# Optimization experiments

Measured on AMD Instinct MI355X. Metric: run time of the kernel, lower is better.

Reference implementation:

```python
import jax, jax.numpy as jnp
import numpy as np
from jax import lax

G = 32          # growthrate / num_features
KS = 3          # filter_size
PAD = (KS - 1) // 2
NUM_LAYERS = 4


def _conv2d(x, w, b):
    # x: [B, Cin, H, W], w: [Cout, Cin, k, k]
    y = lax.conv_general_dilated(
        x, w, window_strides=(1, 1), padding=[(PAD, PAD), (PAD, PAD)],
        dimension_numbers=("NCHW", "OIHW", "NCHW"))
    return y + b[None, :, None, None]


def _scan_cell(xs, w, b):
    # xs: [T, B, Cin, H, W]; ConvLSTM-like cell: A = tanh(conv(cat(x, c)))
    # split A -> (ai[G], af[G], ao[1]); h = ai; c_next = sigmoid(ao) * af
    T, B, _, H, W = xs.shape
    c0 = jnp.zeros((B, G, H, W), xs.dtype)

    def step(c, x):
        A = jnp.tanh(_conv2d(jnp.concatenate([x, c], axis=1), w, b))
        h = A[:, :G]
        cand = A[:, G:2 * G]
        gate = jax.nn.sigmoid(A[:, 2 * G:])
        c_next = gate * cand
        return c_next, (h, c_next, gate)

    _, (hs, cs, gs) = lax.scan(step, c0, xs)
    return hs, cs, gs  # each [T, B, G or 1, H, W]


def setup_inputs() -> dict:
    key = jax.random.key(0)
    ks = jax.random.split(key, 1 + 4 * NUM_LAYERS)
    T, B, C, H, W = 8, 4, 32, 64, 64
    inp = {"x": jax.random.normal(ks[0], (T, B, C, H, W), jnp.float32)}
    cin = [C] + [2 * l * G for l in range(1, NUM_LAYERS)]  # [32, 64, 128, 192]
    cout = 2 * G + 1
    for l in range(NUM_LAYERS):
        ci = cin[l] + G
        inp[f"wf{l}"] = jax.random.normal(ks[1 + 4 * l], (cout, ci, KS, KS), jnp.float32) * 0.02
        inp[f"bf{l}"] = jax.random.normal(ks[2 + 4 * l], (cout,), jnp.float32) * 0.02
        inp[f"wb{l}"] = jax.random.normal(ks[3 + 4 * l], (cout, ci, KS, KS), jnp.float32) * 0.02
        inp[f"bb{l}"] = jax.random.normal(ks[4 + 4 * l], (cout,), jnp.float32) * 0.02
    return inp


def reference(x, wf0, bf0, wb0, bb0, wf1, bf1, wb1, bb1,
              wf2, bf2, wb2, bb2, wf3, bf3, wb3, bb3):
    fwd = [(wf0, bf0), (wf1, bf1), (wf2, bf2), (wf3, bf3)]
    bwd = [(wb0, bb0), (wb1, bb1), (wb2, bb2), (wb3, bb3)]
    output = x  # [T, B, C, H, W]
    lr_h, lr_c, lr_g = [], [], []
    for l in range(NUM_LAYERS):
        hf, cf, gf = _scan_cell(output, *fwd[l])
        hb, _, _ = _scan_cell(output[::-1], *bwd[l])
        hb = hb[::-1]  # align backward pass to original time order
        cur = jnp.concatenate([hf, hb], axis=2)  # [T, B, 2G, H, W]
        output = cur if l == 0 else jnp.concatenate([output, cur], axis=2)
        lr_h.append(hf[-1]); lr_c.append(cf[-1]); lr_g.append(gf[-1])
    return (output, jnp.stack(lr_h), jnp.stack(lr_c), jnp.stack(lr_g))
```

## Files before the change

### kernel.cpp

```cpp
#include <hip/hip_runtime.h>
#include <math.h>

#define T_STEPS 8
#define HW 4096
#define XSTR 192
#define FR_ROW 4352

typedef unsigned short u16;
typedef __attribute__((ext_vector_type(8))) short short8;
typedef __attribute__((ext_vector_type(4))) short short4v;
typedef __attribute__((ext_vector_type(4))) float f32x4;

__device__ __forceinline__ u16 f2bf(float f) {
    unsigned u = __builtin_bit_cast(unsigned, f);
    u += 0x7fffu + ((u >> 16) & 1u);
    return (u16)(u >> 16);
}
__device__ __forceinline__ float bf2f(u16 h) {
    unsigned u = ((unsigned)h) << 16;
    return __builtin_bit_cast(float, u);
}
__device__ __forceinline__ float ftanh(float x) {
    float e = __expf(2.f * x);
    return 1.f - 2.f * __builtin_amdgcn_rcpf(e + 1.f);
}
__device__ __forceinline__ float fsigm(float x) {
    return __builtin_amdgcn_rcpf(1.f + __expf(-x));
}

__global__ __launch_bounds__(256) void transpose_halo(
    const float* __restrict__ src, u16* __restrict__ XT, int src_ctot)
{
    __shared__ float tile[32][257];
    const int img = blockIdx.z;
    const int px0 = blockIdx.x * 256;
    const float* s = src + (size_t)img * src_ctot * HW + px0;
    #pragma unroll
    for (int c = 0; c < 32; ++c)
        tile[c][threadIdx.x] = s[(size_t)c * HW + threadIdx.x];
    __syncthreads();
    const int c = threadIdx.x & 31, pb = threadIdx.x >> 5;
    const int r0 = px0 >> 6;
    for (int p = pb; p < 256; p += 8) {
        int row = r0 + (p >> 6), col = p & 63;
        XT[((size_t)img * 4356 + (row + 1) * 66 + col + 1) * XSTR + c] = f2bf(tile[c][p]);
    }
}

__global__ __launch_bounds__(256) void prep_w(
    const float* __restrict__ wf, const float* __restrict__ wb,
    u16* __restrict__ Wr, int ci_total)
{
    int idx = blockIdx.x * 256 + threadIdx.x;
    int total = 2 * 9 * 80 * ci_total;
    if (idx >= total) return;
    int ci = idx % ci_total;
    int rest = idx / ci_total;
    int co = rest % 80; rest /= 80;
    int tap = rest % 9;
    int dir = rest / 9;
    const float* w = dir ? wb : wf;
    float v = (co < 65) ? w[((size_t)co * ci_total + ci) * 9 + tap] : 0.f;
    Wr[idx] = f2bf(v);
}

__global__ __launch_bounds__(512, 2) void convx_mfma(
    const u16* __restrict__ XT, const u16* __restrict__ Wr,
    const float* __restrict__ b_f, const float* __restrict__ b_b,
    u16* __restrict__ convx, int cin, int ci_total)
{
    __shared__ u16 xs[6 * 66 * 32];
    const int tid = threadIdx.x;
    const int l = tid & 63, wv = tid >> 6;
    const int g = l >> 4, ln16 = l & 15;
    const int img = blockIdx.z;
    const int dir = wv & 1;
    const int wrow = wv >> 1;
    const int r0  = blockIdx.x * 4;
    const int orow = r0 + wrow;

    const float* bias = dir ? b_b : b_f;
    f32x4 acc[5][4];
    #pragma unroll
    for (int mt = 0; mt < 5; ++mt)
        #pragma unroll
        for (int r = 0; r < 4; ++r) {
            int co = mt * 16 + g * 4 + r;
            float bv = (co < 65) ? bias[co] : 0.f;
            #pragma unroll
            for (int nt = 0; nt < 4; ++nt) acc[mt][nt][r] = bv;
        }

    const u16* wdir = Wr + (size_t)dir * 9 * 80 * ci_total + g * 8;
    const u16* xim  = XT + (size_t)img * 4356 * XSTR;

    for (int ch = 0; ch < cin; ch += 32) {
        __syncthreads();
        #pragma unroll
        for (int k = 0; k < 4; ++k) {
            int idx = k * 512 + tid;
            if (idx < 1584) {
                int seg = idx & 3;
                int pr  = idx >> 2;
                short8 v = *(const short8*)(xim + (size_t)(r0 * 66 + pr) * XSTR + ch + seg * 8);
                *(short8*)(xs + (size_t)idx * 8) = v;
            }
        }
        __syncthreads();

        #pragma unroll
        for (int ky = 0; ky < 3; ++ky) {
            #pragma unroll
            for (int kx = 0; kx < 3; ++kx) {
                const int tap = ky * 3 + kx;
                const u16* xb = xs + ((size_t)((wrow + ky) * 66 + ln16 + kx)) * 32 + g * 8;
                short8 bv0 = *(const short8*)(xb);
                short8 bv1 = *(const short8*)(xb + 16 * 32);
                short8 bv2 = *(const short8*)(xb + 32 * 32);
                short8 bv3 = *(const short8*)(xb + 48 * 32);
                const u16* wb_ = wdir + ((size_t)tap * 80 + ln16) * ci_total + ch;
                #pragma unroll
                for (int mt = 0; mt < 5; ++mt) {
                    short8 af = *(const short8*)(wb_ + (size_t)mt * 16 * ci_total);
                    acc[mt][0] = __builtin_amdgcn_mfma_f32_16x16x32_bf16(af, bv0, acc[mt][0], 0, 0, 0);
                    acc[mt][1] = __builtin_amdgcn_mfma_f32_16x16x32_bf16(af, bv1, acc[mt][1], 0, 0, 0);
                    acc[mt][2] = __builtin_amdgcn_mfma_f32_16x16x32_bf16(af, bv2, acc[mt][2], 0, 0, 0);
                    acc[mt][3] = __builtin_amdgcn_mfma_f32_16x16x32_bf16(af, bv3, acc[mt][3], 0, 0, 0);
                }
            }
        }
    }

    const int zimg = dir * 32 + img;
    u16* cb = convx + ((size_t)zimg * 64 + orow) * FR_ROW;
    #pragma unroll
    for (int mt = 0; mt < 4; ++mt)
        #pragma unroll
        for (int nt = 0; nt < 4; ++nt) {
            short4v pk;
            #pragma unroll
            for (int r = 0; r < 4; ++r) pk[r] = (short)f2bf(acc[mt][nt][r]);
            *(short4v*)(cb + (size_t)(nt * 4 + mt) * 256 + l * 4) = pk;
        }
    if (g == 0) {
        #pragma unroll
        for (int nt = 0; nt < 4; ++nt) {
            short4v pk;
            #pragma unroll
            for (int r = 0; r < 4; ++r) pk[r] = (short)f2bf(acc[4][nt][r]);
            *(short4v*)(cb + 4096 + nt * 64 + ln16 * 4) = pk;
        }
    }
}

__global__ __launch_bounds__(256) void rec_mfma(
    const u16* __restrict__ cT_in, u16* __restrict__ cT_out,
    const u16* __restrict__ Wr, const u16* __restrict__ convx,
    float* __restrict__ out_t,
    float* __restrict__ lrh, float* __restrict__ lrc, float* __restrict__ lrg,
    u16* __restrict__ XT,
    int cin, int ci_total, int layer, int step)
{
    const int tid = threadIdx.x;
    const int l = tid & 63, wv = tid >> 6;
    const int g = l >> 4, ln16 = l & 15;
    const int z = blockIdx.z;
    const int dir = z >> 2, b = z & 3;
    const int t = dir ? (7 - step) : step;
    const int row  = blockIdx.x * 2 + (wv >> 1);
    const int nb   = (wv & 1) * 2;
    const int col0 = nb * 16;

    const int zimg = dir * 32 + t * 4 + b;
    const u16* cxb = convx + ((size_t)zimg * 64 + row) * FR_ROW;
    f32x4 acc[5][2];
    #pragma unroll
    for (int mt = 0; mt < 4; ++mt)
        #pragma unroll
        for (int nt = 0; nt < 2; ++nt) {
            short4v pk = *(const short4v*)(cxb + (size_t)((nb + nt) * 4 + mt) * 256 + l * 4);
            #pragma unroll
            for (int r = 0; r < 4; ++r) acc[mt][nt][r] = bf2f((u16)pk[r]);
        }
    #pragma unroll
    for (int nt = 0; nt < 2; ++nt) {
        if (g == 0) {
            short4v pk = *(const short4v*)(cxb + 4096 + (nb + nt) * 64 + ln16 * 4);
            #pragma unroll
            for (int r = 0; r < 4; ++r) acc[4][nt][r] = bf2f((u16)pk[r]);
        } else {
            #pragma unroll
            for (int r = 0; r < 4; ++r) acc[4][nt][r] = 0.f;
        }
    }

    const u16* wdir = Wr + (size_t)dir * 9 * 80 * ci_total + cin + g * 8;
    const u16* cim  = cT_in + (size_t)z * 4356 * 32 + g * 8;

    #pragma unroll
    for (int ky = 0; ky < 3; ++ky) {
        #pragma unroll
        for (int kx = 0; kx < 3; ++kx) {
            const int tap = ky * 3 + kx;
            const u16* xb_ = cim + (size_t)((row + ky) * 66 + col0 + ln16 + kx) * 32;
            short8 bv0 = *(const short8*)(xb_);
            short8 bv1 = *(const short8*)(xb_ + 16 * 32);
            const u16* wb_ = wdir + ((size_t)tap * 80 + ln16) * ci_total;
            #pragma unroll
            for (int mt = 0; mt < 5; ++mt) {
                short8 af = *(const short8*)(wb_ + (size_t)mt * 16 * ci_total);
                acc[mt][0] = __builtin_amdgcn_mfma_f32_16x16x32_bf16(af, bv0, acc[mt][0], 0, 0, 0);
                acc[mt][1] = __builtin_amdgcn_mfma_f32_16x16x32_bf16(af, bv1, acc[mt][1], 0, 0, 0);
            }
        }
    }

    const bool last_f = (dir == 0) && (step == 7);
    float val[2], gv[2];
    #pragma unroll
    for (int nt = 0; nt < 2; ++nt) {
        val[nt] = fsigm(ftanh(acc[4][nt][0]));
        gv[nt]  = __shfl(val[nt], ln16);
    }

    const size_t obase = (size_t)(t * 4 + b) * 256 + 64 * layer + dir * 32;
    const int chb = 64 * layer + dir * 32;
    #pragma unroll
    for (int mt = 0; mt < 2; ++mt)
        #pragma unroll
        for (int nt = 0; nt < 2; ++nt) {
            int px = row * 64 + col0 + nt * 16 + ln16;
            short4v pkh;
            #pragma unroll
            for (int r = 0; r < 4; ++r) {
                int co = mt * 16 + g * 4 + r;
                float v = ftanh(acc[mt][nt][r]);
                out_t[(obase + co) * HW + px] = v;
                pkh[r] = (short)f2bf(v);
                if (last_f) lrh[((size_t)(layer * 4 + b) * 32 + co) * HW + px] = v;
            }
            if (layer < 3)
                *(short4v*)(XT + ((size_t)(t * 4 + b) * 4356 + (row + 1) * 66 +
                                  (col0 + nt * 16 + ln16 + 1)) * XSTR + chb + mt * 16 + g * 4) = pkh;
        }
    #pragma unroll
    for (int mt = 2; mt < 4; ++mt)
        #pragma unroll
        for (int nt = 0; nt < 2; ++nt) {
            short4v pk;
            #pragma unroll
            for (int r = 0; r < 4; ++r) {
                int k = (mt - 2) * 16 + g * 4 + r;
                float c = gv[nt] * ftanh(acc[mt][nt][r]);
                pk[r] = (short)f2bf(c);
                if (last_f)
                    lrc[((size_t)(layer * 4 + b) * 32 + k) * HW + row * 64 + col0 + nt * 16 + ln16] = c;
            }
            int colh = col0 + nt * 16 + ln16 + 1;
            *(short4v*)(cT_out + ((size_t)z * 4356 + (row + 1) * 66 + colh) * 32 + (mt - 2) * 16 + g * 4) = pk;
        }
    if (last_f && g == 0) {
        #pragma unroll
        for (int nt = 0; nt < 2; ++nt)
            lrg[(size_t)(layer * 4 + b) * HW + row * 64 + col0 + nt * 16 + ln16] = val[nt];
    }
}

extern "C" void kernel_launch(void* const* d_in, const int* in_sizes, int n_in,
                              void* d_out, int out_size, void* d_ws, size_t ws_size,
                              hipStream_t stream)
{
    const float* x = (const float*)d_in[0];
    float* out = (float*)d_out;
    float* lrh = out + (size_t)33554432;
    float* lrc = lrh + (size_t)2097152;
    float* lrg = lrc + (size_t)2097152;

    char* ws = (char*)d_ws;
    u16* convx = (u16*)ws;
    size_t off = 35651584 + 4096;
    u16* cT_a = (u16*)(ws + off); off += 2230272;
    u16* cT_b = (u16*)(ws + off); off += 2230272;
    u16* XT   = (u16*)(ws + off); off += 53526528;
    u16* Wr   = (u16*)(ws + off);

    hipMemsetAsync(XT, 0, 53526528, stream);
    hipMemsetAsync(cT_b, 0, 2230272, stream);
    transpose_halo<<<dim3(16, 1, 32), 256, 0, stream>>>(x, XT, 32);

    for (int l = 0; l < 4; ++l) {
        const float* wf = (const float*)d_in[1 + 4 * l];
        const float* bf = (const float*)d_in[2 + 4 * l];
        const float* wb = (const float*)d_in[3 + 4 * l];
        const float* bb = (const float*)d_in[4 + 4 * l];
        int cin = (l == 0) ? 32 : 64 * l;
        int ci_total = cin + 32;

        prep_w<<<dim3((2 * 9 * 80 * ci_total + 255) / 256), 256, 0, stream>>>(wf, wb, Wr, ci_total);
        convx_mfma<<<dim3(16, 1, 32), 512, 0, stream>>>(XT, Wr, bf, bb, convx, cin, ci_total);

        hipMemsetAsync(cT_a, 0, 2230272, stream);
        for (int s = 0; s < 8; ++s) {
            const u16* cin_p = (s & 1) ? cT_b : cT_a;
            u16* cout_p      = (s & 1) ? cT_a : cT_b;
            rec_mfma<<<dim3(32, 1, 8), 256, 0, stream>>>(
                cin_p, cout_p, Wr, convx, out, lrh, lrc, lrg, XT, cin, ci_total, l, s);
        }
    }
}
```

Baseline: 616.4 us.

## Batch weight prep, stage two channel chunks per sync, split rec work across waves

```diff
diff --git a/kernel.cpp b/kernel.cpp
--- a/kernel.cpp
+++ b/kernel.cpp
@@ -47,19 +47,24 @@
     }
 }
 
-__global__ __launch_bounds__(256) void prep_w(
-    const float* __restrict__ wf, const float* __restrict__ wb,
-    u16* __restrict__ Wr, int ci_total)
+struct WP { const float* p[8]; };
+
+__global__ __launch_bounds__(256) void prep_w_all(WP wp, u16* __restrict__ Wr)
 {
     int idx = blockIdx.x * 256 + threadIdx.x;
-    int total = 2 * 9 * 80 * ci_total;
-    if (idx >= total) return;
-    int ci = idx % ci_total;
-    int rest = idx / ci_total;
+    if (idx >= 783360) return;
+    const int offs[5] = {0, 92160, 230400, 460800, 783360};
+    const int cit[4]  = {64, 96, 160, 224};
+    int lay = 0;
+    while (idx >= offs[lay + 1]) ++lay;
+    int li = idx - offs[lay];
+    int ci_total = cit[lay];
+    int ci = li % ci_total;
+    int rest = li / ci_total;
     int co = rest % 80; rest /= 80;
     int tap = rest % 9;
     int dir = rest / 9;
-    const float* w = dir ? wb : wf;
+    const float* w = wp.p[lay * 2 + dir];
     float v = (co < 65) ? w[((size_t)co * ci_total + ci) * 9 + tap] : 0.f;
     Wr[idx] = f2bf(v);
 }
@@ -69,7 +74,7 @@
     const float* __restrict__ b_f, const float* __restrict__ b_b,
     u16* __restrict__ convx, int cin, int ci_total)
 {
-    __shared__ u16 xs[6 * 66 * 32];
+    __shared__ u16 xs[2][6 * 66 * 32];
     const int tid = threadIdx.x;
     const int l = tid & 63, wv = tid >> 6;
     const int g = l >> 4, ln16 = l & 15;
@@ -93,39 +98,47 @@
 
     const u16* wdir = Wr + (size_t)dir * 9 * 80 * ci_total + g * 8;
     const u16* xim  = XT + (size_t)img * 4356 * XSTR;
-
-    for (int ch = 0; ch < cin; ch += 32) {
+    const int nstage = (cin >= 64) ? 3168 : 1584;
+
+    for (int ch0 = 0; ch0 < cin; ch0 += 64) {
         __syncthreads();
         #pragma unroll
-        for (int k = 0; k < 4; ++k) {
+        for (int k = 0; k < 7; ++k) {
             int idx = k * 512 + tid;
-            if (idx < 1584) {
-                int seg = idx & 3;
-                int pr  = idx >> 2;
-                short8 v = *(const short8*)(xim + (size_t)(r0 * 66 + pr) * XSTR + ch + seg * 8);
-                *(short8*)(xs + (size_t)idx * 8) = v;
+            if (idx < nstage) {
+                int bufi = (idx >= 1584) ? 1 : 0;
+                int ii = idx - bufi * 1584;
+                int seg = ii & 3, pr = ii >> 2;
+                short8 v = *(const short8*)(xim + (size_t)(r0 * 66 + pr) * XSTR
+                                            + ch0 + bufi * 32 + seg * 8);
+                *(short8*)(xs[bufi] + (size_t)ii * 8) = v;
             }
         }
         __syncthreads();
 
         #pragma unroll
-        for (int ky = 0; ky < 3; ++ky) {
-            #pragma unroll
-            for (int kx = 0; kx < 3; ++kx) {
-                const int tap = ky * 3 + kx;
-                const u16* xb = xs + ((size_t)((wrow + ky) * 66 + ln16 + kx)) * 32 + g * 8;
-                short8 bv0 = *(const short8*)(xb);
-                short8 bv1 = *(const short8*)(xb + 16 * 32);
-                short8 bv2 = *(const short8*)(xb + 32 * 32);
-                short8 bv3 = *(const short8*)(xb + 48 * 32);
-                const u16* wb_ = wdir + ((size_t)tap * 80 + ln16) * ci_total + ch;
+        for (int cc = 0; cc < 2; ++cc) {
+            const int ch = ch0 + cc * 32;
+            if (ch >= cin) break;
+            #pragma unroll
+            for (int ky = 0; ky < 3; ++ky) {
                 #pragma unroll
-                for (int mt = 0; mt < 5; ++mt) {
-                    short8 af = *(const short8*)(wb_ + (size_t)mt * 16 * ci_total);
-                    acc[mt][0] = __builtin_amdgcn_mfma_f32_16x16x32_bf16(af, bv0, acc[mt][0], 0, 0, 0);
-                    acc[mt][1] = __builtin_amdgcn_mfma_f32_16x16x32_bf16(af, bv1, acc[mt][1], 0, 0, 0);
-                    acc[mt][2] = __builtin_amdgcn_mfma_f32_16x16x32_bf16(af, bv2, acc[mt][2], 0, 0, 0);
-                    acc[mt][3] = __builtin_amdgcn_mfma_f32_16x16x32_bf16(af, bv3, acc[mt][3], 0, 0, 0);
+                for (int kx = 0; kx < 3; ++kx) {
+                    const int tap = ky * 3 + kx;
+                    const u16* xb = xs[cc] + ((size_t)((wrow + ky) * 66 + ln16 + kx)) * 32 + g * 8;
+                    short8 bv0 = *(const short8*)(xb);
+                    short8 bv1 = *(const short8*)(xb + 16 * 32);
+                    short8 bv2 = *(const short8*)(xb + 32 * 32);
+                    short8 bv3 = *(const short8*)(xb + 48 * 32);
+                    const u16* wb_ = wdir + ((size_t)tap * 80 + ln16) * ci_total + ch;
+                    #pragma unroll
+                    for (int mt = 0; mt < 5; ++mt) {
+                        short8 af = *(const short8*)(wb_ + (size_t)mt * 16 * ci_total);
+                        acc[mt][0] = __builtin_amdgcn_mfma_f32_16x16x32_bf16(af, bv0, acc[mt][0], 0, 0, 0);
+                        acc[mt][1] = __builtin_amdgcn_mfma_f32_16x16x32_bf16(af, bv1, acc[mt][1], 0, 0, 0);
+                        acc[mt][2] = __builtin_amdgcn_mfma_f32_16x16x32_bf16(af, bv2, acc[mt][2], 0, 0, 0);
+                        acc[mt][3] = __builtin_amdgcn_mfma_f32_16x16x32_bf16(af, bv3, acc[mt][3], 0, 0, 0);
+                    }
                 }
             }
         }
@@ -153,7 +166,7 @@
     }
 }
 
-__global__ __launch_bounds__(256) void rec_mfma(
+__global__ __launch_bounds__(512) void rec_mfma(
     const u16* __restrict__ cT_in, u16* __restrict__ cT_out,
     const u16* __restrict__ Wr, const u16* __restrict__ convx,
     float* __restrict__ out_t,
@@ -162,107 +175,118 @@
     int cin, int ci_total, int layer, int step)
 {
     const int tid = threadIdx.x;
-    const int l = tid & 63, wv = tid >> 6;
+    const int l = tid & 63, w = tid >> 6;
     const int g = l >> 4, ln16 = l & 15;
+    const int role = w & 1, ws = w >> 1;
     const int z = blockIdx.z;
     const int dir = z >> 2, b = z & 3;
     const int t = dir ? (7 - step) : step;
-    const int row  = blockIdx.x * 2 + (wv >> 1);
-    const int nb   = (wv & 1) * 2;
+    const int row  = blockIdx.x * 2 + (ws >> 1);
+    const int nb   = (ws & 1) * 2;
     const int col0 = nb * 16;
-
     const int zimg = dir * 32 + t * 4 + b;
+    const int m0 = role * 2;
+
     const u16* cxb = convx + ((size_t)zimg * 64 + row) * FR_ROW;
-    f32x4 acc[5][2];
-    #pragma unroll
-    for (int mt = 0; mt < 4; ++mt)
+    f32x4 acc[3][2];
+    #pragma unroll
+    for (int j = 0; j < 2; ++j)
         #pragma unroll
         for (int nt = 0; nt < 2; ++nt) {
-            short4v pk = *(const short4v*)(cxb + (size_t)((nb + nt) * 4 + mt) * 256 + l * 4);
-            #pragma unroll
-            for (int r = 0; r < 4; ++r) acc[mt][nt][r] = bf2f((u16)pk[r]);
+            short4v pk = *(const short4v*)(cxb + (size_t)((nb + nt) * 4 + (m0 + j)) * 256 + l * 4);
+            #pragma unroll
+            for (int r = 0; r < 4; ++r) acc[j][nt][r] = bf2f((u16)pk[r]);
         }
     #pragma unroll
     for (int nt = 0; nt < 2; ++nt) {
         if (g == 0) {
             short4v pk = *(const short4v*)(cxb + 4096 + (nb + nt) * 64 + ln16 * 4);
             #pragma unroll
-            for (int r = 0; r < 4; ++r) acc[4][nt][r] = bf2f((u16)pk[r]);
+            for (int r = 0; r < 4; ++r) acc[2][nt][r] = bf2f((u16)pk[r]);
         } else {
             #pragma unroll
-            for (int r = 0; r < 4; ++r) acc[4][nt][r] = 0.f;
-        }
-    }
-
-    const u16* wdir = Wr + (size_t)dir * 9 * 80 * ci_total + cin + g * 8;
-    const u16* cim  = cT_in + (size_t)z * 4356 * 32 + g * 8;
-
-    #pragma unroll
-    for (int ky = 0; ky < 3; ++ky) {
-        #pragma unroll
-        for (int kx = 0; kx < 3; ++kx) {
-            const int tap = ky * 3 + kx;
-            const u16* xb_ = cim + (size_t)((row + ky) * 66 + col0 + ln16 + kx) * 32;
-            short8 bv0 = *(const short8*)(xb_);
-            short8 bv1 = *(const short8*)(xb_ + 16 * 32);
-            const u16* wb_ = wdir + ((size_t)tap * 80 + ln16) * ci_total;
-            #pragma unroll
-            for (int mt = 0; mt < 5; ++mt) {
-                short8 af = *(const short8*)(wb_ + (size_t)mt * 16 * ci_total);
-                acc[mt][0] = __builtin_amdgcn_mfma_f32_16x16x32_bf16(af, bv0, acc[mt][0], 0, 0, 0);
-                acc[mt][1] = __builtin_amdgcn_mfma_f32_16x16x32_bf16(af, bv1, acc[mt][1], 0, 0, 0);
-            }
-        }
+            for (int r = 0; r < 4; ++r) acc[2][nt][r] = 0.f;
+        }
+    }
+
+    if (step > 0) {
+        const u16* wdir = Wr + (size_t)dir * 9 * 80 * ci_total + cin + g * 8;
+        const u16* cim  = cT_in + (size_t)z * 4356 * 32 + g * 8;
+        __builtin_amdgcn_s_setprio(1);
+        #pragma unroll
+        for (int ky = 0; ky < 3; ++ky) {
+            #pragma unroll
+            for (int kx = 0; kx < 3; ++kx) {
+                const int tap = ky * 3 + kx;
+                const u16* xb_ = cim + (size_t)((row + ky) * 66 + col0 + ln16 + kx) * 32;
+                short8 bv0 = *(const short8*)(xb_);
+                short8 bv1 = *(const short8*)(xb_ + 16 * 32);
+                const u16* wb_ = wdir + ((size_t)tap * 80 + ln16) * ci_total;
+                short8 af0 = *(const short8*)(wb_ + (size_t)(m0    ) * 16 * ci_total);
+                short8 af1 = *(const short8*)(wb_ + (size_t)(m0 + 1) * 16 * ci_total);
+                short8 af4 = *(const short8*)(wb_ + (size_t)4 * 16 * ci_total);
+                acc[0][0] = __builtin_amdgcn_mfma_f32_16x16x32_bf16(af0, bv0, acc[0][0], 0, 0, 0);
+                acc[0][1] = __builtin_amdgcn_mfma_f32_16x16x32_bf16(af0, bv1, acc[0][1], 0, 0, 0);
+                acc[1][0] = __builtin_amdgcn_mfma_f32_16x16x32_bf16(af1, bv0, acc[1][0], 0, 0, 0);
+                acc[1][1] = __builtin_amdgcn_mfma_f32_16x16x32_bf16(af1, bv1, acc[1][1], 0, 0, 0);
+                acc[2][0] = __builtin_amdgcn_mfma_f32_16x16x32_bf16(af4, bv0, acc[2][0], 0, 0, 0);
+                acc[2][1] = __builtin_amdgcn_mfma_f32_16x16x32_bf16(af4, bv1, acc[2][1], 0, 0, 0);
+            }
+        }
+        __builtin_amdgcn_s_setprio(0);
     }
 
     const bool last_f = (dir == 0) && (step == 7);
     float val[2], gv[2];
     #pragma unroll
     for (int nt = 0; nt < 2; ++nt) {
-        val[nt] = fsigm(ftanh(acc[4][nt][0]));
+        val[nt] = fsigm(ftanh(acc[2][nt][0]));
         gv[nt]  = __shfl(val[nt], ln16);
     }
 
-    const size_t obase = (size_t)(t * 4 + b) * 256 + 64 * layer + dir * 32;
-    const int chb = 64 * layer + dir * 32;
-    #pragma unroll
-    for (int mt = 0; mt < 2; ++mt)
-        #pragma unroll
-        for (int nt = 0; nt < 2; ++nt) {
-            int px = row * 64 + col0 + nt * 16 + ln16;
-            short4v pkh;
-            #pragma unroll
-            for (int r = 0; r < 4; ++r) {
-                int co = mt * 16 + g * 4 + r;
-                float v = ftanh(acc[mt][nt][r]);
-                out_t[(obase + co) * HW + px] = v;
-                pkh[r] = (short)f2bf(v);
-                if (last_f) lrh[((size_t)(layer * 4 + b) * 32 + co) * HW + px] = v;
-            }
-            if (layer < 3)
-                *(short4v*)(XT + ((size_t)(t * 4 + b) * 4356 + (row + 1) * 66 +
-                                  (col0 + nt * 16 + ln16 + 1)) * XSTR + chb + mt * 16 + g * 4) = pkh;
-        }
-    #pragma unroll
-    for (int mt = 2; mt < 4; ++mt)
-        #pragma unroll
-        for (int nt = 0; nt < 2; ++nt) {
-            short4v pk;
-            #pragma unroll
-            for (int r = 0; r < 4; ++r) {
-                int k = (mt - 2) * 16 + g * 4 + r;
-                float c = gv[nt] * ftanh(acc[mt][nt][r]);
-                pk[r] = (short)f2bf(c);
-                if (last_f)
-                    lrc[((size_t)(layer * 4 + b) * 32 + k) * HW + row * 64 + col0 + nt * 16 + ln16] = c;
-            }
-            int colh = col0 + nt * 16 + ln16 + 1;
-            *(short4v*)(cT_out + ((size_t)z * 4356 + (row + 1) * 66 + colh) * 32 + (mt - 2) * 16 + g * 4) = pk;
-        }
-    if (last_f && g == 0) {
-        #pragma unroll
-        for (int nt = 0; nt < 2; ++nt)
-            lrg[(size_t)(layer * 4 + b) * HW + row * 64 + col0 + nt * 16 + ln16] = val[nt];
+    if (role == 0) {
+        const size_t obase = (size_t)(t * 4 + b) * 256 + 64 * layer + dir * 32;
+        const int chb = 64 * layer + dir * 32;
+        #pragma unroll
+        for (int j = 0; j < 2; ++j)
+            #pragma unroll
+            for (int nt = 0; nt < 2; ++nt) {
+                int px = row * 64 + col0 + nt * 16 + ln16;
+                short4v pkh;
+                #pragma unroll
+                for (int r = 0; r < 4; ++r) {
+                    int co = j * 16 + g * 4 + r;
+                    float v = ftanh(acc[j][nt][r]);
+                    out_t[(obase + co) * HW + px] = v;
+                    pkh[r] = (short)f2bf(v);
+                    if (last_f) lrh[((size_t)(layer * 4 + b) * 32 + co) * HW + px] = v;
+                }
+                if (layer < 3)
+                    *(short4v*)(XT + ((size_t)(t * 4 + b) * 4356 + (row + 1) * 66 +
+                                      (col0 + nt * 16 + ln16 + 1)) * XSTR + chb + j * 16 + g * 4) = pkh;
+            }
+        if (last_f && g == 0) {
+            #pragma unroll
+            for (int nt = 0; nt < 2; ++nt)
+                lrg[(size_t)(layer * 4 + b) * HW + row * 64 + col0 + nt * 16 + ln16] = val[nt];
+        }
+    } else {
+        #pragma unroll
+        for (int j = 0; j < 2; ++j)
+            #pragma unroll
+            for (int nt = 0; nt < 2; ++nt) {
+                short4v pk;
+                #pragma unroll
+                for (int r = 0; r < 4; ++r) {
+                    int k = j * 16 + g * 4 + r;
+                    float c = gv[nt] * ftanh(acc[j][nt][r]);
+                    pk[r] = (short)f2bf(c);
+                    if (last_f)
+                        lrc[((size_t)(layer * 4 + b) * 32 + k) * HW + row * 64 + col0 + nt * 16 + ln16] = c;
+                }
+                int colh = col0 + nt * 16 + ln16 + 1;
+                *(short4v*)(cT_out + ((size_t)z * 4356 + (row + 1) * 66 + colh) * 32 + j * 16 + g * 4) = pk;
+            }
     }
 }
 
@@ -281,30 +305,38 @@
     size_t off = 35651584 + 4096;
     u16* cT_a = (u16*)(ws + off); off += 2230272;
     u16* cT_b = (u16*)(ws + off); off += 2230272;
-    u16* XT   = (u16*)(ws + off); off += 53526528;
-    u16* Wr   = (u16*)(ws + off);
+    u16* XT = (u16*)(ws + off); off += 53526528;
+    u16* Wr = (u16*)(ws + off);
+
+    static const int offs[4] = {0, 92160, 230400, 460800};
 
     hipMemsetAsync(XT, 0, 53526528, stream);
+    hipMemsetAsync(cT_a, 0, 2230272, stream);
     hipMemsetAsync(cT_b, 0, 2230272, stream);
     transpose_halo<<<dim3(16, 1, 32), 256, 0, stream>>>(x, XT, 32);
 
+    WP wp;
     for (int l = 0; l < 4; ++l) {
-        const float* wf = (const float*)d_in[1 + 4 * l];
+        wp.p[l * 2]     = (const float*)d_in[1 + 4 * l];
+        wp.p[l * 2 + 1] = (const float*)d_in[3 + 4 * l];
+    }
+    prep_w_all<<<dim3((783360 + 255) / 256), 256, 0, stream>>>(wp, Wr);
+
+    for (int l = 0; l < 4; ++l) {
         const float* bf = (const float*)d_in[2 + 4 * l];
-        const float* wb = (const float*)d_in[3 + 4 * l];
         const float* bb = (const float*)d_in[4 + 4 * l];
         int cin = (l == 0) ? 32 : 64 * l;
         int ci_total = cin + 32;
-
-        prep_w<<<dim3((2 * 9 * 80 * ci_total + 255) / 256), 256, 0, stream>>>(wf, wb, Wr, ci_total);
-        convx_mfma<<<dim3(16, 1, 32), 512, 0, stream>>>(XT, Wr, bf, bb, convx, cin, ci_total);
-
-        hipMemsetAsync(cT_a, 0, 2230272, stream);
+        const u16* Wrl = Wr + offs[l];
+
+        convx_mfma<<<dim3(16, 1, 32), 512, 0, stream>>>(XT, Wrl, bf, bb, convx, cin, ci_total);
+
         for (int s = 0; s < 8; ++s) {
             const u16* cin_p = (s & 1) ? cT_b : cT_a;
             u16* cout_p      = (s & 1) ? cT_a : cT_b;
-            rec_mfma<<<dim3(32, 1, 8), 256, 0, stream>>>(
-                cin_p, cout_p, Wr, convx, out, lrh, lrc, lrg, XT, cin, ci_total, l, s);
-        }
-    }
-}
+            rec_mfma<<<dim3(32, 1, 8), 512, 0, stream>>>(
+                cin_p, cout_p, Wrl, convx, out, lrh, lrc, lrg, XT,
+                cin, ci_total, l, s);
+        }
+    }
+}
```

After: 668.1 us. 1.08x slower.
